# Performance work log

Measured on AMD Instinct MI355X. Metric: run time of the kernel, lower is better.

## Reference

```python
import jax, jax.numpy as jnp
import numpy as np

N_A, N_P = 50000, 100000          # author / paper node counts
E_W, E_C = 1600000, 3200000       # writes & written_by edges, cites edges
NEG_SLOPE = 0.2                   # DGL GATConv default leaky_relu slope
EPS = 1e-12                       # F.normalize eps


def _gat(h_src, h_dst, src, dst, W, al, ar, b, n_dst):
    """DGL GATConv: fc -> per-head additive attention -> edge softmax -> weighted sum + bias."""
    H, F = al.shape
    fs = (h_src @ W.T).reshape(-1, H, F)            # [Ns, H, F]
    fd = (h_dst @ W.T).reshape(-1, H, F)            # [Nd, H, F]
    el = (fs * al).sum(-1)                          # [Ns, H]
    er = (fd * ar).sum(-1)                          # [Nd, H]
    e = jax.nn.leaky_relu(el[src] + er[dst], NEG_SLOPE)      # [E, H]
    m = jax.lax.stop_gradient(jax.ops.segment_max(e, dst, num_segments=n_dst))
    ex = jnp.exp(e - m[dst])
    s = jax.ops.segment_sum(ex, dst, num_segments=n_dst)
    a = ex / s[dst]                                 # edge softmax per dst node, per head
    rst = jax.ops.segment_sum(fs[src] * a[:, :, None], dst, num_segments=n_dst)
    return rst + b.reshape(H, F)                    # [Nd, H, F]


def _l2norm(x):
    return x / jnp.maximum(jnp.linalg.norm(x, axis=1, keepdims=True), EPS)


def setup_inputs() -> dict:
    key = jax.random.key(0)
    ks = iter(jax.random.split(key, 64))
    def nrm(shape, scale=0.1):
        return jax.random.normal(next(ks), shape, dtype=jnp.float32) * scale
    inp = {
        'feat_author': jax.random.normal(next(ks), (N_A, 128), dtype=jnp.float32),
        'feat_paper':  jax.random.normal(next(ks), (N_P, 256), dtype=jnp.float32),
        'fm_W_author': nrm((64, 128)), 'fm_b_author': nrm((64,)),
        'fm_W_paper':  nrm((64, 256)), 'fm_b_paper':  nrm((64,)),
    }
    for e in ('writes', 'written_by', 'cites'):
        inp[f'g1_{e}_W'] = nrm((64, 64)); inp[f'g1_{e}_al'] = nrm((4, 16))
        inp[f'g1_{e}_ar'] = nrm((4, 16)); inp[f'g1_{e}_b'] = nrm((64,))
        inp[f'g2_{e}_W'] = nrm((64, 64)); inp[f'g2_{e}_al'] = nrm((1, 64))
        inp[f'g2_{e}_ar'] = nrm((1, 64)); inp[f'g2_{e}_b'] = nrm((64,))
    inp['w_src'] = jax.random.randint(next(ks), (E_W,), 0, N_A, dtype=jnp.int32)
    inp['w_dst'] = jax.random.randint(next(ks), (E_W,), 0, N_P, dtype=jnp.int32)
    inp['wb_src'] = jax.random.randint(next(ks), (E_W,), 0, N_P, dtype=jnp.int32)
    inp['wb_dst'] = jax.random.randint(next(ks), (E_W,), 0, N_A, dtype=jnp.int32)
    inp['c_src'] = jax.random.randint(next(ks), (E_C,), 0, N_P, dtype=jnp.int32)
    inp['c_dst'] = jax.random.randint(next(ks), (E_C,), 0, N_P, dtype=jnp.int32)
    return inp


def reference(feat_author, feat_paper, fm_W_author, fm_b_author, fm_W_paper, fm_b_paper,
              g1_writes_W, g1_writes_al, g1_writes_ar, g1_writes_b,
              g2_writes_W, g2_writes_al, g2_writes_ar, g2_writes_b,
              g1_written_by_W, g1_written_by_al, g1_written_by_ar, g1_written_by_b,
              g2_written_by_W, g2_written_by_al, g2_written_by_ar, g2_written_by_b,
              g1_cites_W, g1_cites_al, g1_cites_ar, g1_cites_b,
              g2_cites_W, g2_cites_al, g2_cites_ar, g2_cites_b,
              w_src, w_dst, wb_src, wb_dst, c_src, c_dst):
    # FeatureMappingLayer: per-ntype Linear -> relu, out_dim 64
    h_a = jax.nn.relu(feat_author @ fm_W_author.T + fm_b_author)
    h_p = jax.nn.relu(feat_paper @ fm_W_paper.T + fm_b_paper)
    # NodeAttentionLayer: per-etype GATConv(64 -> 16, 4 heads), flatten, sum over incoming etypes
    h1_p = (_gat(h_a, h_p, w_src, w_dst, g1_writes_W, g1_writes_al, g1_writes_ar, g1_writes_b, N_P)
            + _gat(h_p, h_p, c_src, c_dst, g1_cites_W, g1_cites_al, g1_cites_ar, g1_cites_b, N_P)
           ).reshape(N_P, 64)
    h1_a = _gat(h_p, h_a, wb_src, wb_dst, g1_written_by_W, g1_written_by_al, g1_written_by_ar,
                g1_written_by_b, N_A).reshape(N_A, 64)
    # gat2: per-etype GATConv(64 -> 64, 1 head) on h1[:, :64] (== h1), squeeze, sum
    h2_p = (_gat(h1_a, h1_p, w_src, w_dst, g2_writes_W, g2_writes_al, g2_writes_ar, g2_writes_b, N_P)
            + _gat(h1_p, h1_p, c_src, c_dst, g2_cites_W, g2_cites_al, g2_cites_ar, g2_cites_b, N_P)
           ).reshape(N_P, 64)
    h2_a = _gat(h1_p, h1_a, wb_src, wb_dst, g2_written_by_W, g2_written_by_al, g2_written_by_ar,
                g2_written_by_b, N_A).reshape(N_A, 64)
    # F.normalize(p=2, dim=1)
    return (_l2norm(h2_a), _l2norm(h2_p))
```

## Files before the change

kernel.cpp:

```cpp
#include <hip/hip_runtime.h>
#include <hip/hip_bf16.h>

#define N_A 50000
#define N_P 100000
#define E_W 1600000
#define E_C 3200000
#define HA (N_A*64)
#define HP (N_P*64)

typedef __attribute__((ext_vector_type(8))) short short8_t;
typedef __attribute__((ext_vector_type(4))) float f32x4;

__device__ __forceinline__ unsigned short f2b(float f)
{
    __hip_bfloat16 b = __float2bfloat16(f);
    return *reinterpret_cast<unsigned short*>(&b);
}

__global__ __launch_bounds__(256) void gemm_mfma(const float* __restrict__ X,
        const float* __restrict__ W, const float* __restrict__ bias,
        void* __restrict__ out, int M, int K, int doRelu, int outBf16)
{
    __shared__ unsigned short Xs[128][72];
    __shared__ unsigned short Wsh[64][72];
    int tid = threadIdx.x, lane = tid & 63, wv = tid >> 6;
    int row0 = blockIdx.x * 128;
    int m = lane & 15, kb = lane >> 4;

    f32x4 acc[2][4];
#pragma unroll
    for (int rb = 0; rb < 2; ++rb)
#pragma unroll
        for (int cb = 0; cb < 4; ++cb) acc[rb][cb] = (f32x4){0.f, 0.f, 0.f, 0.f};

    for (int k0 = 0; k0 < K; k0 += 64) {
        {
            int rbase = (tid >> 4) * 8;
            int c4 = (tid & 15) * 4;
#pragma unroll
            for (int i = 0; i < 8; ++i) {
                int rg = row0 + rbase + i; if (rg >= M) rg = M - 1;
                float4 v = *reinterpret_cast<const float4*>(&X[(long)rg * K + k0 + c4]);
                Xs[rbase + i][c4 + 0] = f2b(v.x);
                Xs[rbase + i][c4 + 1] = f2b(v.y);
                Xs[rbase + i][c4 + 2] = f2b(v.z);
                Xs[rbase + i][c4 + 3] = f2b(v.w);
            }
            int wr = tid >> 2;
            int wc = (tid & 3) * 16;
#pragma unroll
            for (int q = 0; q < 4; ++q) {
                float4 v = *reinterpret_cast<const float4*>(&W[(long)wr * K + k0 + wc + q * 4]);
                Wsh[wr][wc + q * 4 + 0] = f2b(v.x);
                Wsh[wr][wc + q * 4 + 1] = f2b(v.y);
                Wsh[wr][wc + q * 4 + 2] = f2b(v.z);
                Wsh[wr][wc + q * 4 + 3] = f2b(v.w);
            }
        }
        __syncthreads();
#pragma unroll
        for (int kc = 0; kc < 2; ++kc) {
            short8_t a0 = *reinterpret_cast<const short8_t*>(&Xs[wv * 32 + m][kc * 32 + kb * 8]);
            short8_t a1 = *reinterpret_cast<const short8_t*>(&Xs[wv * 32 + 16 + m][kc * 32 + kb * 8]);
#pragma unroll
            for (int cb = 0; cb < 4; ++cb) {
                short8_t b = *reinterpret_cast<const short8_t*>(&Wsh[cb * 16 + m][kc * 32 + kb * 8]);
                acc[0][cb] = __builtin_amdgcn_mfma_f32_16x16x32_bf16(a0, b, acc[0][cb], 0, 0, 0);
                acc[1][cb] = __builtin_amdgcn_mfma_f32_16x16x32_bf16(a1, b, acc[1][cb], 0, 0, 0);
            }
        }
        __syncthreads();
    }

#pragma unroll
    for (int rb = 0; rb < 2; ++rb)
#pragma unroll
    for (int j = 0; j < 4; ++j) {
        int r = row0 + wv * 32 + rb * 16 + (lane >> 4) * 4 + j;
        if (r < M) {
#pragma unroll
            for (int cb = 0; cb < 4; ++cb) {
                int c = cb * 16 + m;
                float v = acc[rb][cb][j];
                if (bias) v += bias[c];
                if (doRelu) v = fmaxf(v, 0.f);
                if (outBf16) ((unsigned short*)out)[(long)r * 64 + c] = f2b(v);
                else         ((float*)out)[(long)r * 64 + c] = v;
            }
        }
    }
}

struct PA { const float* W; const float* a; float* o; int H; };
__global__ void prep_attn12(PA p0, PA p1, PA p2, PA p3, PA p4, PA p5,
                            PA p6, PA p7, PA p8, PA p9, PA p10, PA p11)
{
    PA p;
    switch (blockIdx.x) {
        case 0: p = p0; break;  case 1: p = p1; break;  case 2: p = p2; break;
        case 3: p = p3; break;  case 4: p = p4; break;  case 5: p = p5; break;
        case 6: p = p6; break;  case 7: p = p7; break;  case 8: p = p8; break;
        case 9: p = p9; break;  case 10: p = p10; break; default: p = p11; break;
    }
    int k = threadIdx.x;
    int F = 64 / p.H;
    for (int hh = 0; hh < p.H; ++hh) {
        float s = 0.f;
        for (int f = 0; f < F; ++f)
            s = fmaf(p.W[(hh * F + f) * 64 + k], p.a[hh * F + f], s);
        p.o[k * p.H + hh] = s;
    }
}

__global__ __launch_bounds__(256) void attnvec_mat(
        const float* __restrict__ hP, int NPn,
        const float* __restrict__ fP0, float* __restrict__ oP0,
        const float* __restrict__ fP1, float* __restrict__ oP1,
        const float* __restrict__ fP2, float* __restrict__ oP2,
        const float* __restrict__ fP3, float* __restrict__ oP3,
        const float* __restrict__ hA, int NAn,
        const float* __restrict__ fA0, float* __restrict__ oA0,
        const float* __restrict__ fA1, float* __restrict__ oA1,
        int H, int hb)
{
    __shared__ float hs[64 * 66];
    int tid = threadIdx.x;
    int slotsP = (H == 4) ? 16 : 4;
    int npbP = 256 / slotsP;
    int blocksP = (NPn + npbP - 1) / npbP;

    const float* hsrc; int node0, npb, slots, ncols, N;
    const float* fv0; const float* fv1; const float* fv2; const float* fv3;
    float* ov0; float* ov1; float* ov2; float* ov3;
    if ((int)blockIdx.x < blocksP) {
        hsrc = hP; N = NPn; slots = slotsP; npb = npbP;
        node0 = blockIdx.x * npb;
        ncols = 4 * H;
        fv0 = fP0; ov0 = oP0; fv1 = fP1; ov1 = oP1;
        fv2 = fP2; ov2 = oP2; fv3 = fP3; ov3 = oP3;
    } else {
        int b = (int)blockIdx.x - blocksP;
        hsrc = hA; N = NAn;
        slots = (H == 4) ? 8 : 4; npb = 256 / slots;
        node0 = b * npb;
        ncols = 2 * H;
        fv0 = fA0; ov0 = oA0; fv1 = fA1; ov1 = oA1;
        fv2 = fA0; ov2 = oA0; fv3 = fA1; ov3 = oA1;
    }

    for (int idx = tid; idx < npb * 64; idx += 256) {
        int row = idx >> 6, k = idx & 63;
        int g = node0 + row; if (g >= N) g = N - 1;
        hs[row * 66 + k] = hsrc[(long)g * 64 + k];
    }
    __syncthreads();

    int sshift = (slots == 16) ? 4 : (slots == 8) ? 3 : 2;
    int nl = tid >> sshift;
    int c = tid & (slots - 1);
    int node = node0 + nl;
    if (node >= N || c >= ncols || nl >= npb) return;
    int f = c >> hb;
    int hh = c & (H - 1);
    const float* fv = (f == 0) ? fv0 : (f == 1) ? fv1 : (f == 2) ? fv2 : fv3;
    float* ov = (f == 0) ? ov0 : (f == 1) ? ov1 : (f == 2) ? ov2 : ov3;

    float s = 0.f;
    const float* hrow = &hs[nl * 66];
#pragma unroll 8
    for (int k = 0; k < 64; ++k)
        s = fmaf(hrow[k], fv[k * H + hh], s);
    ov[(long)node * H + hh] = s;
}

__global__ void bucket_hist3(const int* __restrict__ d0, int E0, int* __restrict__ b0,
                             const int* __restrict__ d1, int E1, int* __restrict__ b1,
                             const int* __restrict__ d2, int E2, int* __restrict__ b2,
                             int shift, int blocksPer)
{
    int g = blockIdx.x / blocksPer, bb = blockIdx.x - g * blocksPer;
    const int* dst = g == 0 ? d0 : g == 1 ? d1 : d2;
    int E = g == 0 ? E0 : g == 1 ? E1 : E2;
    int* bcnt = g == 0 ? b0 : g == 1 ? b1 : b2;
    __shared__ int h[256];
    int tid = threadIdx.x;
    h[tid] = 0;
    __syncthreads();
    for (long i = (long)bb * 256 + tid; i < E; i += (long)blocksPer * 256)
        atomicAdd(&h[dst[i] >> shift], 1);
    __syncthreads();
    if (h[tid]) atomicAdd(&bcnt[tid], h[tid]);
}

__global__ void bucket_scan3(int* __restrict__ bcnt, int* __restrict__ bstart,
                             int* __restrict__ gcur,
                             int* __restrict__ o0, int Nn0, int Ee0,
                             int* __restrict__ o1, int Nn1, int Ee1,
                             int* __restrict__ o2, int Nn2, int Ee2)
{
    int g = blockIdx.x;
    int* bc = bcnt + g * 256;
    int* bs = bstart + g * 257;
    int* gc = gcur + g * 256;
    int* offs = g == 0 ? o0 : g == 1 ? o1 : o2;
    int N = g == 0 ? Nn0 : g == 1 ? Nn1 : Nn2;
    int E = g == 0 ? Ee0 : g == 1 ? Ee1 : Ee2;
    __shared__ int sc[256];
    int tid = threadIdx.x;
    int v = bc[tid];
    sc[tid] = v;
    __syncthreads();
    for (int off = 1; off < 256; off <<= 1) {
        int t = (tid >= off) ? sc[tid - off] : 0;
        __syncthreads();
        sc[tid] += t;
        __syncthreads();
    }
    int excl = sc[tid] - v;
    bs[tid] = excl;
    gc[tid] = excl;
    if (tid == 255) bs[256] = E;
    if (tid == 0) offs[N] = E;
}

#define EPT 8
__global__ __launch_bounds__(256) void part_kernel(const int* __restrict__ src,
        const int* __restrict__ dst, int* __restrict__ gcur,
        uint2* __restrict__ pairs, int E, int NB, int shift)
{
    __shared__ int hcnt[256];
    __shared__ int hbase[256];
    int tid = threadIdx.x;
    long base = (long)blockIdx.x * (256 * EPT);
    for (int i = tid; i < NB; i += 256) hcnt[i] = 0;
    __syncthreads();
    int b[EPT], r[EPT], s[EPT], d[EPT];
#pragma unroll
    for (int k = 0; k < EPT; ++k) {
        long idx = base + k * 256 + tid;
        if (idx < E) {
            s[k] = src[idx]; d[k] = dst[idx];
            b[k] = d[k] >> shift;
            r[k] = atomicAdd(&hcnt[b[k]], 1);
        } else b[k] = -1;
    }
    __syncthreads();
    for (int i = tid; i < NB; i += 256) {
        if (hcnt[i]) hbase[i] = atomicAdd(&gcur[i], hcnt[i]);
    }
    __syncthreads();
#pragma unroll
    for (int k = 0; k < EPT; ++k) {
        if (b[k] >= 0)
            pairs[hbase[b[k]] + r[k]] = make_uint2((unsigned)s[k], (unsigned)d[k]);
    }
}

__global__ __launch_bounds__(512) void csr_finalize(const uint2* __restrict__ pairs,
        const int* __restrict__ bstart, int* __restrict__ offs, int* __restrict__ csr,
        int N, int shift)
{
    __shared__ int cnt[512];
    __shared__ int sc[512];
    int tid = threadIdx.x;
    int b = blockIdx.x;
    int d0 = b << shift;
    int pS = bstart[b], pE = bstart[b + 1];
    cnt[tid] = 0;
    __syncthreads();
    for (int i = pS + tid; i < pE; i += 512)
        atomicAdd(&cnt[pairs[i].y - d0], 1);
    __syncthreads();
    int v = cnt[tid];
    sc[tid] = v;
    __syncthreads();
    for (int off = 1; off < 512; off <<= 1) {
        int t = (tid >= off) ? sc[tid - off] : 0;
        __syncthreads();
        sc[tid] += t;
        __syncthreads();
    }
    int excl = sc[tid] - v;
    if (d0 + tid < N) offs[d0 + tid] = pS + excl;
    cnt[tid] = excl;
    __syncthreads();
    for (int i = pS + tid; i < pE; i += 512) {
        uint2 u = pairs[i];
        int p = atomicAdd(&cnt[u.y - d0], 1);
        csr[pS + p] = (int)u.x;
    }
}

__global__ void gat_csr_kernel(const int* __restrict__ offs, const int* __restrict__ csr,
                               const float* __restrict__ el, const float* __restrict__ er,
                               const unsigned short* __restrict__ Fsrc, float* __restrict__ rst,
                               int Nd, int hshift,
                               const float* __restrict__ bias0, const float* __restrict__ bias1)
{
    int d = (blockIdx.x << 2) | (threadIdx.x >> 6);
    int lane = threadIdx.x & 63;
    if (d >= Nd) return;
    int H = 1 << hshift;
    int off = offs[d];
    int n = offs[d + 1] - off;
    int g8 = lane >> 3;
    int fo = (lane & 7) * 8;
    int hf = (hshift == 2) ? ((lane & 7) >> 1) : 0;

    if (n == 0) {
        if (bias0 && lane < 8) {
            float4 o0, o1;
            o0.x = bias0[fo + 0]; o0.y = bias0[fo + 1]; o0.z = bias0[fo + 2]; o0.w = bias0[fo + 3];
            o1.x = bias0[fo + 4]; o1.y = bias0[fo + 5]; o1.z = bias0[fo + 6]; o1.w = bias0[fo + 7];
            if (bias1) {
                o0.x += bias1[fo + 0]; o0.y += bias1[fo + 1]; o0.z += bias1[fo + 2]; o0.w += bias1[fo + 3];
                o1.x += bias1[fo + 4]; o1.y += bias1[fo + 5]; o1.z += bias1[fo + 6]; o1.w += bias1[fo + 7];
            }
            *reinterpret_cast<float4*>(&rst[(long)d * 64 + fo]) = o0;
            *reinterpret_cast<float4*>(&rst[(long)d * 64 + fo + 4]) = o1;
        }
        return;
    }

    int h = lane & (H - 1);
    float erd = er[d * H + h];
    int estep = 64 >> hshift;
    float acc[8];
#pragma unroll
    for (int q = 0; q < 8; ++q) acc[q] = 0.f;
    float ssum = 0.f;

    for (int base = 0; base < n; base += estep) {
        int i = base + (lane >> hshift);
        int sn = 0; float a = 0.f;
        if (i < n) {
            sn = csr[off + i];
            float v = el[sn * H + h] + erd;
            v = v > 0.f ? v : 0.2f * v;
            a = __expf(v);
            ssum += a;
        }
        int rounds = min(estep, n - base);
#pragma unroll 2
        for (int r = 0; r * 8 < rounds; ++r) {
            int sl = r * 8 + g8;
            int lsn = sl << hshift;
            int s2 = __shfl(sn, lsn, 64);
            float a2 = __shfl(a, lsn | hf, 64);
            uint4 u = *reinterpret_cast<const uint4*>(&Fsrc[(long)s2 * 64 + fo]);
            acc[0] = fmaf(__uint_as_float(u.x << 16), a2, acc[0]);
            acc[1] = fmaf(__uint_as_float(u.x & 0xffff0000u), a2, acc[1]);
            acc[2] = fmaf(__uint_as_float(u.y << 16), a2, acc[2]);
            acc[3] = fmaf(__uint_as_float(u.y & 0xffff0000u), a2, acc[3]);
            acc[4] = fmaf(__uint_as_float(u.z << 16), a2, acc[4]);
            acc[5] = fmaf(__uint_as_float(u.z & 0xffff0000u), a2, acc[5]);
            acc[6] = fmaf(__uint_as_float(u.w << 16), a2, acc[6]);
            acc[7] = fmaf(__uint_as_float(u.w & 0xffff0000u), a2, acc[7]);
        }
    }

    for (int o = H; o < 64; o <<= 1) ssum += __shfl_xor(ssum, o, 64);
    float rinv = 1.f / __shfl(ssum, hf, 64);

#pragma unroll
    for (int q = 0; q < 8; ++q) {
        acc[q] += __shfl_xor(acc[q], 8, 64);
        acc[q] += __shfl_xor(acc[q], 16, 64);
        acc[q] += __shfl_xor(acc[q], 32, 64);
    }
    if (lane < 8) {
        float4 o0, o1;
        if (bias0) {
            o0.x = bias0[fo + 0]; o0.y = bias0[fo + 1]; o0.z = bias0[fo + 2]; o0.w = bias0[fo + 3];
            o1.x = bias0[fo + 4]; o1.y = bias0[fo + 5]; o1.z = bias0[fo + 6]; o1.w = bias0[fo + 7];
            if (bias1) {
                o0.x += bias1[fo + 0]; o0.y += bias1[fo + 1]; o0.z += bias1[fo + 2]; o0.w += bias1[fo + 3];
                o1.x += bias1[fo + 4]; o1.y += bias1[fo + 5]; o1.z += bias1[fo + 6]; o1.w += bias1[fo + 7];
            }
        } else {
            o0 = *reinterpret_cast<float4*>(&rst[(long)d * 64 + fo]);
            o1 = *reinterpret_cast<float4*>(&rst[(long)d * 64 + fo + 4]);
        }
        o0.x = fmaf(acc[0], rinv, o0.x); o0.y = fmaf(acc[1], rinv, o0.y);
        o0.z = fmaf(acc[2], rinv, o0.z); o0.w = fmaf(acc[3], rinv, o0.w);
        o1.x = fmaf(acc[4], rinv, o1.x); o1.y = fmaf(acc[5], rinv, o1.y);
        o1.z = fmaf(acc[6], rinv, o1.z); o1.w = fmaf(acc[7], rinv, o1.w);
        *reinterpret_cast<float4*>(&rst[(long)d * 64 + fo]) = o0;
        *reinterpret_cast<float4*>(&rst[(long)d * 64 + fo + 4]) = o1;
    }
}

__global__ void l2norm2(const float* __restrict__ inA, const float* __restrict__ inP,
                        float* __restrict__ out, int NAn, int NPn)
{
    long gt = (long)blockIdx.x * blockDim.x + threadIdx.x;
    int row = (int)(gt >> 6);
    int lane = threadIdx.x & 63;
    if (row >= NAn + NPn) return;
    float v = (row < NAn) ? inA[(long)row * 64 + lane]
                          : inP[(long)(row - NAn) * 64 + lane];
    float ss = v * v;
    for (int off = 1; off < 64; off <<= 1) ss += __shfl_xor(ss, off, 64);
    out[(long)row * 64 + lane] = v / fmaxf(sqrtf(ss), 1e-12f);
}

extern "C" void kernel_launch(void* const* d_in, const int* in_sizes, int n_in,
                              void* d_out, int out_size, void* d_ws, size_t ws_size,
                              hipStream_t stream)
{
    const float* feat_a = (const float*)d_in[0];
    const float* feat_p = (const float*)d_in[1];
    const float* fmWa = (const float*)d_in[2];
    const float* fmba = (const float*)d_in[3];
    const float* fmWp = (const float*)d_in[4];
    const float* fmbp = (const float*)d_in[5];
    const float* g1w_W = (const float*)d_in[6];  const float* g1w_al = (const float*)d_in[7];
    const float* g1w_ar = (const float*)d_in[8]; const float* g1w_b = (const float*)d_in[9];
    const float* g2w_W = (const float*)d_in[10]; const float* g2w_al = (const float*)d_in[11];
    const float* g2w_ar = (const float*)d_in[12]; const float* g2w_b = (const float*)d_in[13];
    const float* g1wb_W = (const float*)d_in[14]; const float* g1wb_al = (const float*)d_in[15];
    const float* g1wb_ar = (const float*)d_in[16]; const float* g1wb_b = (const float*)d_in[17];
    const float* g2wb_W = (const float*)d_in[18]; const float* g2wb_al = (const float*)d_in[19];
    const float* g2wb_ar = (const float*)d_in[20]; const float* g2wb_b = (const float*)d_in[21];
    const float* g1c_W = (const float*)d_in[22]; const float* g1c_al = (const float*)d_in[23];
    const float* g1c_ar = (const float*)d_in[24]; const float* g1c_b = (const float*)d_in[25];
    const float* g2c_W = (const float*)d_in[26]; const float* g2c_al = (const float*)d_in[27];
    const float* g2c_ar = (const float*)d_in[28]; const float* g2c_b = (const float*)d_in[29];
    const int* w_src = (const int*)d_in[30];
    const int* w_dst = (const int*)d_in[31];
    const int* wb_src = (const int*)d_in[32];
    const int* wb_dst = (const int*)d_in[33];
    const int* c_src = (const int*)d_in[34];
    const int* c_dst = (const int*)d_in[35];

    float* ws = (float*)d_ws;
    size_t off = 0;
    auto alloc = [&](size_t n) { float* p = ws + off; off += n; return p; };
    float* h_a  = alloc(HA);
    float* h_p  = alloc(HP);
    unsigned short* Pa = (unsigned short*)alloc(HP / 2 + 16);
    float* h1_p = alloc(HP);
    float* h1_a = alloc(HA);
    float* el_w  = alloc((size_t)N_A * 4);
    float* er_w  = alloc((size_t)N_P * 4);
    float* el_c  = alloc((size_t)N_P * 4);
    float* er_c  = alloc((size_t)N_P * 4);
    float* el_wb = alloc((size_t)N_P * 4);
    float* er_wb = alloc((size_t)N_A * 4);
    float* fold  = alloc(12 * 256);
    int* w_offs  = (int*)alloc(N_P + 1);
    int* c_offs  = (int*)alloc(N_P + 1);
    int* wb_offs = (int*)alloc(N_A + 1);
    int* bcnt3   = (int*)alloc(3 * 256);
    int* bstart3 = (int*)alloc(3 * 257);
    int* gcur3   = (int*)alloc(3 * 256);
    int* w_csr   = (int*)alloc(E_W);
    int* c_csr   = (int*)alloc(E_C);
    int* wb_csr  = (int*)alloc(E_W);
    off = (off + 1) & ~(size_t)1;
    uint2* pairs = (uint2*)alloc((size_t)E_C * 2);
    float* h2_p = h_p;
    float* h2_a = h_a;

    float* wal_w1 = fold + 0*256,  *war_w1 = fold + 1*256;
    float* wal_c1 = fold + 2*256,  *war_c1 = fold + 3*256;
    float* wal_b1 = fold + 4*256,  *war_b1 = fold + 5*256;
    float* wal_w2 = fold + 6*256,  *war_w2 = fold + 7*256;
    float* wal_c2 = fold + 8*256,  *war_c2 = fold + 9*256;
    float* wal_b2 = fold + 10*256, *war_b2 = fold + 11*256;

    const int SHIFT = 9;
    int NB_P = (N_P + 511) >> 9;
    int NB_A = (N_A + 511) >> 9;

    hipMemsetAsync(bcnt3, 0, 3 * 256 * sizeof(int), stream);
    bucket_hist3<<<3 * 256, 256, 0, stream>>>(w_dst, E_W, bcnt3,
                                              c_dst, E_C, bcnt3 + 256,
                                              wb_dst, E_W, bcnt3 + 512, SHIFT, 256);
    bucket_scan3<<<3, 256, 0, stream>>>(bcnt3, bstart3, gcur3,
                                        w_offs, N_P, E_W,
                                        c_offs, N_P, E_C,
                                        wb_offs, N_A, E_W);
    part_kernel<<<(E_W + 2047) / 2048, 256, 0, stream>>>(w_src, w_dst, gcur3, pairs, E_W, NB_P, SHIFT);
    csr_finalize<<<NB_P, 512, 0, stream>>>(pairs, bstart3, w_offs, w_csr, N_P, SHIFT);
    part_kernel<<<(E_C + 2047) / 2048, 256, 0, stream>>>(c_src, c_dst, gcur3 + 256, pairs, E_C, NB_P, SHIFT);
    csr_finalize<<<NB_P, 512, 0, stream>>>(pairs, bstart3 + 257, c_offs, c_csr, N_P, SHIFT);
    part_kernel<<<(E_W + 2047) / 2048, 256, 0, stream>>>(wb_src, wb_dst, gcur3 + 512, pairs, E_W, NB_A, SHIFT);
    csr_finalize<<<NB_A, 512, 0, stream>>>(pairs, bstart3 + 514, wb_offs, wb_csr, N_A, SHIFT);

    prep_attn12<<<12, 64, 0, stream>>>(
        PA{g1w_W,  g1w_al,  wal_w1, 4}, PA{g1w_W,  g1w_ar,  war_w1, 4},
        PA{g1c_W,  g1c_al,  wal_c1, 4}, PA{g1c_W,  g1c_ar,  war_c1, 4},
        PA{g1wb_W, g1wb_al, wal_b1, 4}, PA{g1wb_W, g1wb_ar, war_b1, 4},
        PA{g2w_W,  g2w_al,  wal_w2, 1}, PA{g2w_W,  g2w_ar,  war_w2, 1},
        PA{g2c_W,  g2c_al,  wal_c2, 1}, PA{g2c_W,  g2c_ar,  war_c2, 1},
        PA{g2wb_W, g2wb_al, wal_b2, 1}, PA{g2wb_W, g2wb_ar, war_b2, 1});

    gemm_mfma<<<(N_A + 127) / 128, 256, 0, stream>>>(feat_a, fmWa, fmba, h_a, N_A, 128, 1, 0);
    gemm_mfma<<<(N_P + 127) / 128, 256, 0, stream>>>(feat_p, fmWp, fmbp, h_p, N_P, 256, 1, 0);

    {
        int npbP = 16, npbA = 32;
        int grid = (N_P + npbP - 1) / npbP + (N_A + npbA - 1) / npbA;
        attnvec_mat<<<grid, 256, 0, stream>>>(
            h_p, N_P, wal_c1, el_c, war_c1, er_c, war_w1, er_w, wal_b1, el_wb,
            h_a, N_A, wal_w1, el_w, war_b1, er_wb, 4, 2);
    }
    gemm_mfma<<<(N_A + 127) / 128, 256, 0, stream>>>(h_a, g1w_W, nullptr, Pa, N_A, 64, 0, 1);
    gat_csr_kernel<<<(N_P + 3) / 4, 256, 0, stream>>>(w_offs, w_csr, el_w, er_w, Pa, h1_p,
                                                      N_P, 2, g1w_b, g1c_b);
    gemm_mfma<<<(N_P + 127) / 128, 256, 0, stream>>>(h_p, g1c_W, nullptr, Pa, N_P, 64, 0, 1);
    gat_csr_kernel<<<(N_P + 3) / 4, 256, 0, stream>>>(c_offs, c_csr, el_c, er_c, Pa, h1_p,
                                                      N_P, 2, nullptr, nullptr);
    gemm_mfma<<<(N_P + 127) / 128, 256, 0, stream>>>(h_p, g1wb_W, nullptr, Pa, N_P, 64, 0, 1);
    gat_csr_kernel<<<(N_A + 3) / 4, 256, 0, stream>>>(wb_offs, wb_csr, el_wb, er_wb, Pa, h1_a,
                                                      N_A, 2, g1wb_b, nullptr);

    {
        int npbP = 64, npbA = 64;
        int grid = (N_P + npbP - 1) / npbP + (N_A + npbA - 1) / npbA;
        attnvec_mat<<<grid, 256, 0, stream>>>(
            h1_p, N_P, wal_c2, el_c, war_c2, er_c, war_w2, er_w, wal_b2, el_wb,
            h1_a, N_A, wal_w2, el_w, war_b2, er_wb, 1, 0);
    }
    gemm_mfma<<<(N_A + 127) / 128, 256, 0, stream>>>(h1_a, g2w_W, nullptr, Pa, N_A, 64, 0, 1);
    gat_csr_kernel<<<(N_P + 3) / 4, 256, 0, stream>>>(w_offs, w_csr, el_w, er_w, Pa, h2_p,
                                                      N_P, 0, g2w_b, g2c_b);
    gemm_mfma<<<(N_P + 127) / 128, 256, 0, stream>>>(h1_p, g2c_W, nullptr, Pa, N_P, 64, 0, 1);
    gat_csr_kernel<<<(N_P + 3) / 4, 256, 0, stream>>>(c_offs, c_csr, el_c, er_c, Pa, h2_p,
                                                      N_P, 0, nullptr, nullptr);
    gemm_mfma<<<(N_P + 127) / 128, 256, 0, stream>>>(h1_p, g2wb_W, nullptr, Pa, N_P, 64, 0, 1);
    gat_csr_kernel<<<(N_A + 3) / 4, 256, 0, stream>>>(wb_offs, wb_csr, el_wb, er_wb, Pa, h2_a,
                                                      N_A, 0, g2wb_b, nullptr);

    l2norm2<<<(((long)(N_A + N_P)) * 64 + 255) / 256, 256, 0, stream>>>(
        h2_a, h2_p, (float*)d_out, N_A, N_P);
}
```

Measured before the change: 843.8 us.

## Batch projections and fuse per-etype GAT aggregation with bias and L2 norm

The two feature-map GEMMs become one launch, and the three per-layer projection GEMMs become one launch writing into separate bf16 buffers. The three per-etype GAT aggregations are merged into one kernel that accumulates both paper etypes in registers. This removes the read-modify-write of the partial result and folds the final L2 normalization into the second layer's epilogue. The aim is fewer launches, less serialization and less global traffic, at the cost of extra workspace for the three projection buffers.

```diff
diff --git a/kernel.cpp b/kernel.cpp
--- a/kernel.cpp
+++ b/kernel.cpp
@@ -17,14 +17,22 @@
     return *reinterpret_cast<unsigned short*>(&b);
 }
 
-__global__ __launch_bounds__(256) void gemm_mfma(const float* __restrict__ X,
-        const float* __restrict__ W, const float* __restrict__ bias,
-        void* __restrict__ out, int M, int K, int doRelu, int outBf16)
+__global__ __launch_bounds__(256) void gemm_fm2(
+        const float* __restrict__ X0, const float* __restrict__ W0,
+        const float* __restrict__ b0, float* __restrict__ out0, int M0, int K0, int nb0,
+        const float* __restrict__ X1, const float* __restrict__ W1,
+        const float* __restrict__ b1, float* __restrict__ out1, int M1, int K1)
 {
     __shared__ unsigned short Xs[128][72];
     __shared__ unsigned short Wsh[64][72];
+    const float *X, *W, *bias; float* out; int M, K, row0;
+    if ((int)blockIdx.x < nb0) {
+        X = X0; W = W0; bias = b0; out = out0; M = M0; K = K0; row0 = blockIdx.x * 128;
+    } else {
+        X = X1; W = W1; bias = b1; out = out1; M = M1; K = K1;
+        row0 = ((int)blockIdx.x - nb0) * 128;
+    }
     int tid = threadIdx.x, lane = tid & 63, wv = tid >> 6;
-    int row0 = blockIdx.x * 128;
     int m = lane & 15, kb = lane >> 4;
 
     f32x4 acc[2][4];
@@ -34,28 +42,26 @@
         for (int cb = 0; cb < 4; ++cb) acc[rb][cb] = (f32x4){0.f, 0.f, 0.f, 0.f};
 
     for (int k0 = 0; k0 < K; k0 += 64) {
-        {
-            int rbase = (tid >> 4) * 8;
-            int c4 = (tid & 15) * 4;
-#pragma unroll
-            for (int i = 0; i < 8; ++i) {
-                int rg = row0 + rbase + i; if (rg >= M) rg = M - 1;
-                float4 v = *reinterpret_cast<const float4*>(&X[(long)rg * K + k0 + c4]);
-                Xs[rbase + i][c4 + 0] = f2b(v.x);
-                Xs[rbase + i][c4 + 1] = f2b(v.y);
-                Xs[rbase + i][c4 + 2] = f2b(v.z);
-                Xs[rbase + i][c4 + 3] = f2b(v.w);
-            }
-            int wr = tid >> 2;
-            int wc = (tid & 3) * 16;
-#pragma unroll
-            for (int q = 0; q < 4; ++q) {
-                float4 v = *reinterpret_cast<const float4*>(&W[(long)wr * K + k0 + wc + q * 4]);
-                Wsh[wr][wc + q * 4 + 0] = f2b(v.x);
-                Wsh[wr][wc + q * 4 + 1] = f2b(v.y);
-                Wsh[wr][wc + q * 4 + 2] = f2b(v.z);
-                Wsh[wr][wc + q * 4 + 3] = f2b(v.w);
-            }
+        int rbase = (tid >> 4) * 8;
+        int c4 = (tid & 15) * 4;
+#pragma unroll
+        for (int i = 0; i < 8; ++i) {
+            int rg = row0 + rbase + i; if (rg >= M) rg = M - 1;
+            float4 v = *reinterpret_cast<const float4*>(&X[(long)rg * K + k0 + c4]);
+            Xs[rbase + i][c4 + 0] = f2b(v.x);
+            Xs[rbase + i][c4 + 1] = f2b(v.y);
+            Xs[rbase + i][c4 + 2] = f2b(v.z);
+            Xs[rbase + i][c4 + 3] = f2b(v.w);
+        }
+        int wr = tid >> 2;
+        int wc = (tid & 3) * 16;
+#pragma unroll
+        for (int q = 0; q < 4; ++q) {
+            float4 v = *reinterpret_cast<const float4*>(&W[(long)wr * K + k0 + wc + q * 4]);
+            Wsh[wr][wc + q * 4 + 0] = f2b(v.x);
+            Wsh[wr][wc + q * 4 + 1] = f2b(v.y);
+            Wsh[wr][wc + q * 4 + 2] = f2b(v.z);
+            Wsh[wr][wc + q * 4 + 3] = f2b(v.w);
         }
         __syncthreads();
 #pragma unroll
@@ -81,12 +87,82 @@
 #pragma unroll
             for (int cb = 0; cb < 4; ++cb) {
                 int c = cb * 16 + m;
-                float v = acc[rb][cb][j];
-                if (bias) v += bias[c];
-                if (doRelu) v = fmaxf(v, 0.f);
-                if (outBf16) ((unsigned short*)out)[(long)r * 64 + c] = f2b(v);
-                else         ((float*)out)[(long)r * 64 + c] = v;
+                float v = acc[rb][cb][j] + bias[c];
+                out[(long)r * 64 + c] = fmaxf(v, 0.f);
             }
+        }
+    }
+}
+
+__global__ __launch_bounds__(256) void proj3(
+        const float* __restrict__ X0, const float* __restrict__ W0,
+        unsigned short* __restrict__ o0, int M0, int nb0,
+        const float* __restrict__ X1, const float* __restrict__ W1,
+        unsigned short* __restrict__ o1, int M1, int nb1,
+        const float* __restrict__ X2, const float* __restrict__ W2,
+        unsigned short* __restrict__ o2, int M2)
+{
+    __shared__ unsigned short Xs[128][72];
+    __shared__ unsigned short Wsh[64][72];
+    const float *X, *W; unsigned short* out; int M, row0;
+    if ((int)blockIdx.x < nb0) {
+        X = X0; W = W0; out = o0; M = M0; row0 = blockIdx.x * 128;
+    } else if ((int)blockIdx.x < nb0 + nb1) {
+        X = X1; W = W1; out = o1; M = M1; row0 = ((int)blockIdx.x - nb0) * 128;
+    } else {
+        X = X2; W = W2; out = o2; M = M2; row0 = ((int)blockIdx.x - nb0 - nb1) * 128;
+    }
+    int tid = threadIdx.x, lane = tid & 63, wv = tid >> 6;
+    int m = lane & 15, kb = lane >> 4;
+
+    int rbase = (tid >> 4) * 8;
+    int c4 = (tid & 15) * 4;
+#pragma unroll
+    for (int i = 0; i < 8; ++i) {
+        int rg = row0 + rbase + i; if (rg >= M) rg = M - 1;
+        float4 v = *reinterpret_cast<const float4*>(&X[(long)rg * 64 + c4]);
+        Xs[rbase + i][c4 + 0] = f2b(v.x);
+        Xs[rbase + i][c4 + 1] = f2b(v.y);
+        Xs[rbase + i][c4 + 2] = f2b(v.z);
+        Xs[rbase + i][c4 + 3] = f2b(v.w);
+    }
+    int wr = tid >> 2;
+    int wc = (tid & 3) * 16;
+#pragma unroll
+    for (int q = 0; q < 4; ++q) {
+        float4 v = *reinterpret_cast<const float4*>(&W[(long)wr * 64 + wc + q * 4]);
+        Wsh[wr][wc + q * 4 + 0] = f2b(v.x);
+        Wsh[wr][wc + q * 4 + 1] = f2b(v.y);
+        Wsh[wr][wc + q * 4 + 2] = f2b(v.z);
+        Wsh[wr][wc + q * 4 + 3] = f2b(v.w);
+    }
+    __syncthreads();
+
+    f32x4 acc[2][4];
+#pragma unroll
+    for (int rb = 0; rb < 2; ++rb)
+#pragma unroll
+        for (int cb = 0; cb < 4; ++cb) acc[rb][cb] = (f32x4){0.f, 0.f, 0.f, 0.f};
+#pragma unroll
+    for (int kc = 0; kc < 2; ++kc) {
+        short8_t a0 = *reinterpret_cast<const short8_t*>(&Xs[wv * 32 + m][kc * 32 + kb * 8]);
+        short8_t a1 = *reinterpret_cast<const short8_t*>(&Xs[wv * 32 + 16 + m][kc * 32 + kb * 8]);
+#pragma unroll
+        for (int cb = 0; cb < 4; ++cb) {
+            short8_t b = *reinterpret_cast<const short8_t*>(&Wsh[cb * 16 + m][kc * 32 + kb * 8]);
+            acc[0][cb] = __builtin_amdgcn_mfma_f32_16x16x32_bf16(a0, b, acc[0][cb], 0, 0, 0);
+            acc[1][cb] = __builtin_amdgcn_mfma_f32_16x16x32_bf16(a1, b, acc[1][cb], 0, 0, 0);
+        }
+    }
+#pragma unroll
+    for (int rb = 0; rb < 2; ++rb)
+#pragma unroll
+    for (int j = 0; j < 4; ++j) {
+        int r = row0 + wv * 32 + rb * 16 + (lane >> 4) * 4 + j;
+        if (r < M) {
+#pragma unroll
+            for (int cb = 0; cb < 4; ++cb)
+                out[(long)r * 64 + cb * 16 + m] = f2b(acc[rb][cb][j]);
         }
     }
 }
@@ -291,37 +367,18 @@
     }
 }
 
-__global__ void gat_csr_kernel(const int* __restrict__ offs, const int* __restrict__ csr,
-                               const float* __restrict__ el, const float* __restrict__ er,
-                               const unsigned short* __restrict__ Fsrc, float* __restrict__ rst,
-                               int Nd, int hshift,
-                               const float* __restrict__ bias0, const float* __restrict__ bias1)
-{
-    int d = (blockIdx.x << 2) | (threadIdx.x >> 6);
-    int lane = threadIdx.x & 63;
-    if (d >= Nd) return;
+__device__ __forceinline__ void gat_graph(int d, const int* __restrict__ offs,
+        const int* __restrict__ csr, const float* __restrict__ el,
+        const float* __restrict__ er, const unsigned short* __restrict__ P,
+        int hshift, int lane, float* o)
+{
     int H = 1 << hshift;
     int off = offs[d];
     int n = offs[d + 1] - off;
+    if (n == 0) return;
     int g8 = lane >> 3;
     int fo = (lane & 7) * 8;
     int hf = (hshift == 2) ? ((lane & 7) >> 1) : 0;
-
-    if (n == 0) {
-        if (bias0 && lane < 8) {
-            float4 o0, o1;
-            o0.x = bias0[fo + 0]; o0.y = bias0[fo + 1]; o0.z = bias0[fo + 2]; o0.w = bias0[fo + 3];
-            o1.x = bias0[fo + 4]; o1.y = bias0[fo + 5]; o1.z = bias0[fo + 6]; o1.w = bias0[fo + 7];
-            if (bias1) {
-                o0.x += bias1[fo + 0]; o0.y += bias1[fo + 1]; o0.z += bias1[fo + 2]; o0.w += bias1[fo + 3];
-                o1.x += bias1[fo + 4]; o1.y += bias1[fo + 5]; o1.z += bias1[fo + 6]; o1.w += bias1[fo + 7];
-            }
-            *reinterpret_cast<float4*>(&rst[(long)d * 64 + fo]) = o0;
-            *reinterpret_cast<float4*>(&rst[(long)d * 64 + fo + 4]) = o1;
-        }
-        return;
-    }
-
     int h = lane & (H - 1);
     float erd = er[d * H + h];
     int estep = 64 >> hshift;
@@ -347,7 +404,7 @@
             int lsn = sl << hshift;
             int s2 = __shfl(sn, lsn, 64);
             float a2 = __shfl(a, lsn | hf, 64);
-            uint4 u = *reinterpret_cast<const uint4*>(&Fsrc[(long)s2 * 64 + fo]);
+            uint4 u = *reinterpret_cast<const uint4*>(&P[(long)s2 * 64 + fo]);
             acc[0] = fmaf(__uint_as_float(u.x << 16), a2, acc[0]);
             acc[1] = fmaf(__uint_as_float(u.x & 0xffff0000u), a2, acc[1]);
             acc[2] = fmaf(__uint_as_float(u.y << 16), a2, acc[2]);
@@ -359,49 +416,74 @@
         }
     }
 
-    for (int o = H; o < 64; o <<= 1) ssum += __shfl_xor(ssum, o, 64);
+    for (int oo = H; oo < 64; oo <<= 1) ssum += __shfl_xor(ssum, oo, 64);
     float rinv = 1.f / __shfl(ssum, hf, 64);
-
 #pragma unroll
     for (int q = 0; q < 8; ++q) {
         acc[q] += __shfl_xor(acc[q], 8, 64);
         acc[q] += __shfl_xor(acc[q], 16, 64);
         acc[q] += __shfl_xor(acc[q], 32, 64);
+        o[q] = fmaf(acc[q], rinv, o[q]);
+    }
+}
+
+__global__ void gat_fused(
+        int NPn, const int* __restrict__ w_offs, const int* __restrict__ w_csr,
+        const float* __restrict__ el_w, const float* __restrict__ er_w,
+        const unsigned short* __restrict__ Pw,
+        const int* __restrict__ c_offs, const int* __restrict__ c_csr,
+        const float* __restrict__ el_c, const float* __restrict__ er_c,
+        const unsigned short* __restrict__ Pc,
+        const float* __restrict__ bP0, const float* __restrict__ bP1,
+        float* __restrict__ outP,
+        int NAn, const int* __restrict__ wb_offs, const int* __restrict__ wb_csr,
+        const float* __restrict__ el_wb, const float* __restrict__ er_wb,
+        const unsigned short* __restrict__ Pwb,
+        const float* __restrict__ bA0, float* __restrict__ outA,
+        int hshift, int doNorm)
+{
+    int blocksP = (NPn + 3) >> 2;
+    int lane = threadIdx.x & 63;
+    int sub = threadIdx.x >> 6;
+    int fo = (lane & 7) * 8;
+    float o[8];
+    float* dst;
+
+    if ((int)blockIdx.x < blocksP) {
+        int d = ((int)blockIdx.x << 2) | sub;
+        if (d >= NPn) return;
+#pragma unroll
+        for (int q = 0; q < 8; ++q) o[q] = bP0[fo + q] + bP1[fo + q];
+        gat_graph(d, w_offs, w_csr, el_w, er_w, Pw, hshift, lane, o);
+        gat_graph(d, c_offs, c_csr, el_c, er_c, Pc, hshift, lane, o);
+        dst = outP + (long)d * 64;
+    } else {
+        int d = (((int)blockIdx.x - blocksP) << 2) | sub;
+        if (d >= NAn) return;
+#pragma unroll
+        for (int q = 0; q < 8; ++q) o[q] = bA0[fo + q];
+        gat_graph(d, wb_offs, wb_csr, el_wb, er_wb, Pwb, hshift, lane, o);
+        dst = outA + (long)d * 64;
+    }
+
+    if (doNorm) {
+        float ss = 0.f;
+#pragma unroll
+        for (int q = 0; q < 8; ++q) ss = fmaf(o[q], o[q], ss);
+        ss += __shfl_xor(ss, 1, 64);
+        ss += __shfl_xor(ss, 2, 64);
+        ss += __shfl_xor(ss, 4, 64);
+        float sc = 1.f / fmaxf(sqrtf(ss), 1e-12f);
+#pragma unroll
+        for (int q = 0; q < 8; ++q) o[q] *= sc;
     }
     if (lane < 8) {
         float4 o0, o1;
-        if (bias0) {
-            o0.x = bias0[fo + 0]; o0.y = bias0[fo + 1]; o0.z = bias0[fo + 2]; o0.w = bias0[fo + 3];
-            o1.x = bias0[fo + 4]; o1.y = bias0[fo + 5]; o1.z = bias0[fo + 6]; o1.w = bias0[fo + 7];
-            if (bias1) {
-                o0.x += bias1[fo + 0]; o0.y += bias1[fo + 1]; o0.z += bias1[fo + 2]; o0.w += bias1[fo + 3];
-                o1.x += bias1[fo + 4]; o1.y += bias1[fo + 5]; o1.z += bias1[fo + 6]; o1.w += bias1[fo + 7];
-            }
-        } else {
-            o0 = *reinterpret_cast<float4*>(&rst[(long)d * 64 + fo]);
-            o1 = *reinterpret_cast<float4*>(&rst[(long)d * 64 + fo + 4]);
-        }
-        o0.x = fmaf(acc[0], rinv, o0.x); o0.y = fmaf(acc[1], rinv, o0.y);
-        o0.z = fmaf(acc[2], rinv, o0.z); o0.w = fmaf(acc[3], rinv, o0.w);
-        o1.x = fmaf(acc[4], rinv, o1.x); o1.y = fmaf(acc[5], rinv, o1.y);
-        o1.z = fmaf(acc[6], rinv, o1.z); o1.w = fmaf(acc[7], rinv, o1.w);
-        *reinterpret_cast<float4*>(&rst[(long)d * 64 + fo]) = o0;
-        *reinterpret_cast<float4*>(&rst[(long)d * 64 + fo + 4]) = o1;
-    }
-}
-
-__global__ void l2norm2(const float* __restrict__ inA, const float* __restrict__ inP,
-                        float* __restrict__ out, int NAn, int NPn)
-{
-    long gt = (long)blockIdx.x * blockDim.x + threadIdx.x;
-    int row = (int)(gt >> 6);
-    int lane = threadIdx.x & 63;
-    if (row >= NAn + NPn) return;
-    float v = (row < NAn) ? inA[(long)row * 64 + lane]
-                          : inP[(long)(row - NAn) * 64 + lane];
-    float ss = v * v;
-    for (int off = 1; off < 64; off <<= 1) ss += __shfl_xor(ss, off, 64);
-    out[(long)row * 64 + lane] = v / fmaxf(sqrtf(ss), 1e-12f);
+        o0.x = o[0]; o0.y = o[1]; o0.z = o[2]; o0.w = o[3];
+        o1.x = o[4]; o1.y = o[5]; o1.z = o[6]; o1.w = o[7];
+        *reinterpret_cast<float4*>(dst + fo) = o0;
+        *reinterpret_cast<float4*>(dst + fo + 4) = o1;
+    }
 }
 
 extern "C" void kernel_launch(void* const* d_in, const int* in_sizes, int n_in,
@@ -438,9 +520,11 @@
     auto alloc = [&](size_t n) { float* p = ws + off; off += n; return p; };
     float* h_a  = alloc(HA);
     float* h_p  = alloc(HP);
-    unsigned short* Pa = (unsigned short*)alloc(HP / 2 + 16);
     float* h1_p = alloc(HP);
     float* h1_a = alloc(HA);
+    unsigned short* Pw  = (unsigned short*)alloc(HA / 2 + 16);
+    unsigned short* Pc  = (unsigned short*)alloc(HP / 2 + 16);
+    unsigned short* Pwb = (unsigned short*)alloc(HP / 2 + 16);
     float* el_w  = alloc((size_t)N_A * 4);
     float* er_w  = alloc((size_t)N_P * 4);
     float* el_c  = alloc((size_t)N_P * 4);
@@ -459,8 +543,6 @@
     int* wb_csr  = (int*)alloc(E_W);
     off = (off + 1) & ~(size_t)1;
     uint2* pairs = (uint2*)alloc((size_t)E_C * 2);
-    float* h2_p = h_p;
-    float* h2_a = h_a;
 
     float* wal_w1 = fold + 0*256,  *war_w1 = fold + 1*256;
     float* wal_c1 = fold + 2*256,  *war_c1 = fold + 3*256;
@@ -496,8 +578,15 @@
         PA{g2c_W,  g2c_al,  wal_c2, 1}, PA{g2c_W,  g2c_ar,  war_c2, 1},
         PA{g2wb_W, g2wb_al, wal_b2, 1}, PA{g2wb_W, g2wb_ar, war_b2, 1});
 
-    gemm_mfma<<<(N_A + 127) / 128, 256, 0, stream>>>(feat_a, fmWa, fmba, h_a, N_A, 128, 1, 0);
-    gemm_mfma<<<(N_P + 127) / 128, 256, 0, stream>>>(feat_p, fmWp, fmbp, h_p, N_P, 256, 1, 0);
+    {
+        int nb0 = (N_A + 127) / 128;
+        int nb1 = (N_P + 127) / 128;
+        gemm_fm2<<<nb0 + nb1, 256, 0, stream>>>(feat_a, fmWa, fmba, h_a, N_A, 128, nb0,
+                                                feat_p, fmWp, fmbp, h_p, N_P, 256);
+    }
+
+    int nbA = (N_A + 127) / 128, nbP = (N_P + 127) / 128;
+    int gatGrid = (N_P + 3) / 4 + (N_A + 3) / 4;
 
     {
         int npbP = 16, npbA = 32;
@@ -506,15 +595,13 @@
             h_p, N_P, wal_c1, el_c, war_c1, er_c, war_w1, er_w, wal_b1, el_wb,
             h_a, N_A, wal_w1, el_w, war_b1, er_wb, 4, 2);
     }
-    gemm_mfma<<<(N_A + 127) / 128, 256, 0, stream>>>(h_a, g1w_W, nullptr, Pa, N_A, 64, 0, 1);
-    gat_csr_kernel<<<(N_P + 3) / 4, 256, 0, stream>>>(w_offs, w_csr, el_w, er_w, Pa, h1_p,
-                                                      N_P, 2, g1w_b, g1c_b);
-    gemm_mfma<<<(N_P + 127) / 128, 256, 0, stream>>>(h_p, g1c_W, nullptr, Pa, N_P, 64, 0, 1);
-    gat_csr_kernel<<<(N_P + 3) / 4, 256, 0, stream>>>(c_offs, c_csr, el_c, er_c, Pa, h1_p,
-                                                      N_P, 2, nullptr, nullptr);
-    gemm_mfma<<<(N_P + 127) / 128, 256, 0, stream>>>(h_p, g1wb_W, nullptr, Pa, N_P, 64, 0, 1);
-    gat_csr_kernel<<<(N_A + 3) / 4, 256, 0, stream>>>(wb_offs, wb_csr, el_wb, er_wb, Pa, h1_a,
-                                                      N_A, 2, g1wb_b, nullptr);
+    proj3<<<nbA + 2 * nbP, 256, 0, stream>>>(h_a, g1w_W, Pw, N_A, nbA,
+                                             h_p, g1c_W, Pc, N_P, nbP,
+                                             h_p, g1wb_W, Pwb, N_P);
+    gat_fused<<<gatGrid, 256, 0, stream>>>(
+        N_P, w_offs, w_csr, el_w, er_w, Pw,
+        c_offs, c_csr, el_c, er_c, Pc, g1w_b, g1c_b, h1_p,
+        N_A, wb_offs, wb_csr, el_wb, er_wb, Pwb, g1wb_b, h1_a, 2, 0);
 
     {
         int npbP = 64, npbA = 64;
@@ -523,16 +610,12 @@
             h1_p, N_P, wal_c2, el_c, war_c2, er_c, war_w2, er_w, wal_b2, el_wb,
             h1_a, N_A, wal_w2, el_w, war_b2, er_wb, 1, 0);
     }
-    gemm_mfma<<<(N_A + 127) / 128, 256, 0, stream>>>(h1_a, g2w_W, nullptr, Pa, N_A, 64, 0, 1);
-    gat_csr_kernel<<<(N_P + 3) / 4, 256, 0, stream>>>(w_offs, w_csr, el_w, er_w, Pa, h2_p,
-                                                      N_P, 0, g2w_b, g2c_b);
-    gemm_mfma<<<(N_P + 127) / 128, 256, 0, stream>>>(h1_p, g2c_W, nullptr, Pa, N_P, 64, 0, 1);
-    gat_csr_kernel<<<(N_P + 3) / 4, 256, 0, stream>>>(c_offs, c_csr, el_c, er_c, Pa, h2_p,
-                                                      N_P, 0, nullptr, nullptr);
-    gemm_mfma<<<(N_P + 127) / 128, 256, 0, stream>>>(h1_p, g2wb_W, nullptr, Pa, N_P, 64, 0, 1);
-    gat_csr_kernel<<<(N_A + 3) / 4, 256, 0, stream>>>(wb_offs, wb_csr, el_wb, er_wb, Pa, h2_a,
-                                                      N_A, 0, g2wb_b, nullptr);
-
-    l2norm2<<<(((long)(N_A + N_P)) * 64 + 255) / 256, 256, 0, stream>>>(
-        h2_a, h2_p, (float*)d_out, N_A, N_P);
-}
+    proj3<<<nbA + 2 * nbP, 256, 0, stream>>>(h1_a, g2w_W, Pw, N_A, nbA,
+                                             h1_p, g2c_W, Pc, N_P, nbP,
+                                             h1_p, g2wb_W, Pwb, N_P);
+    float* out = (float*)d_out;
+    gat_fused<<<gatGrid, 256, 0, stream>>>(
+        N_P, w_offs, w_csr, el_w, er_w, Pw,
+        c_offs, c_csr, el_c, er_c, Pc, g2w_b, g2c_b, out + HA,
+        N_A, wb_offs, wb_csr, el_wb, er_wb, Pwb, g2wb_b, out, 0, 1);
+}
```

After: 785.6 us. 1.07x faster.
